# Kernel optimization log

Hardware: AMD Instinct MI355X
Metric: run time of the kernel (lower is better)

## Reference

```python
import jax, jax.numpy as jnp
import numpy as np

B, E, S, D = 32, 64, 50, 300   # batch, sentences/essay, words/sentence, word dim
F = 100                        # conv filters (cnn_lstm_convunits_size)
H = 100                        # lstm units (cnn_lstm_att_pool_size)
W_WIN = 5                      # word window length


def setup_inputs() -> dict:
    key = jax.random.key(0)
    ks = jax.random.split(key, 12)
    n = lambda k, shape: (jax.random.normal(k, shape, jnp.float32) * 0.05)
    return {
        "essays": jax.random.normal(ks[0], (B, E, S, D), jnp.float32),
        "conv_k": n(ks[1], (1, W_WIN, D, F)),      # HWIO
        "conv_b": jnp.zeros((F,), jnp.float32),
        "att1_mat": n(ks[2], (F, F)),
        "att1_bias": n(ks[3], (F,)),
        "att1_vec": n(ks[4], (F, 1)),
        "lstm_W": n(ks[5], (F + H, 4 * H)),        # TF BasicLSTMCell kernel, gate order i,j,f,o
        "lstm_b": jnp.zeros((4 * H,), jnp.float32),
        "att2_mat": n(ks[6], (H, H)),
        "att2_bias": n(ks[7], (H,)),
        "att2_vec": n(ks[8], (H, 1)),
        "dense_w": n(ks[9], (H, 1)),
        "dense_b": jnp.zeros((1,), jnp.float32),
    }


def reference(essays, conv_k, conv_b, att1_mat, att1_bias, att1_vec,
              lstm_W, lstm_b, att2_mat, att2_bias, att2_vec,
              dense_w, dense_b):
    # conv2d, kernel [1, w_window_len], SAME padding, relu  -> [B,E,S,F]
    conv1 = jax.lax.conv_general_dilated(
        essays, conv_k, window_strides=(1, 1), padding="SAME",
        dimension_numbers=("NHWC", "HWIO", "NHWC"))
    conv1 = jax.nn.relu(conv1 + conv_b)

    # attention pooling over words (axis=2)
    a1 = jnp.tanh(jnp.einsum("besf,fg->besg", conv1, att1_mat) + att1_bias)
    a1 = jnp.einsum("besg,go->beso", a1, att1_vec)          # [B,E,S,1]
    a1 = jax.nn.softmax(a1, axis=2)
    sent = jnp.sum(a1 * conv1, axis=2)                       # [B,E,F]

    # BasicLSTMCell (forget_bias=1.0, gate order i,j,f,o) over sentence axis
    hdim = lstm_b.shape[0] // 4
    bsz = essays.shape[0]

    def step(carry, xt):
        c, h = carry
        z = jnp.concatenate([xt, h], axis=1) @ lstm_W + lstm_b
        i, j, f, o = jnp.split(z, 4, axis=1)
        c = c * jax.nn.sigmoid(f + 1.0) + jax.nn.sigmoid(i) * jnp.tanh(j)
        h = jax.nn.sigmoid(o) * jnp.tanh(c)
        return (c, h), h

    init = (jnp.zeros((bsz, hdim), sent.dtype), jnp.zeros((bsz, hdim), sent.dtype))
    xs = jnp.swapaxes(sent, 0, 1)                            # [E,B,F]
    _, hs = jax.lax.scan(step, init, xs)
    lstm = jnp.swapaxes(hs, 0, 1)                            # [B,E,H]

    # attention pooling over sentences (axis=1)
    a2 = jnp.tanh(jnp.einsum("beh,hg->beg", lstm, att2_mat) + att2_bias)
    a2 = jnp.einsum("beg,go->beo", a2, att2_vec)             # [B,E,1]
    a2 = jax.nn.softmax(a2, axis=1)
    essay_repr = jnp.sum(a2 * lstm, axis=1)                  # [B,H]

    preds = jax.nn.sigmoid(essay_repr @ dense_w + dense_b).reshape(-1)  # [B]
    return preds
```

## Files before the change

kernel.cpp:

```cpp
#include <hip/hip_runtime.h>
#include <hip/hip_bf16.h>
#include <stdint.h>

#define Bsz 32
#define Esz 64
#define Ssz 50
#define Dsz 300
#define Fsz 100
#define Hsz 100
#define WWIN 5

#define PX   328
#define PC   136
#define KT_CONV 50
#define NTILES  7
#define MTILES  4
#define NGRP 2214

typedef __attribute__((ext_vector_type(8))) short bf16x8;
typedef __attribute__((ext_vector_type(8))) unsigned short u16x8;
typedef __attribute__((ext_vector_type(4))) float f32x4;
typedef _Float16 half2_t __attribute__((ext_vector_type(2)));

union UH32 { unsigned int u; half2_t v; };
union UH16 { _Float16 h; unsigned short u; };

__device__ __forceinline__ float sigmoid_fast(float x) {
    return 1.0f / (1.0f + __expf(-x));
}
__device__ __forceinline__ float tanhf_fast(float x) {
    const float ax = fabsf(x);
    const float e = __expf(2.0f * ax);
    const float t = 1.0f - 2.0f / (e + 1.0f);
    return copysignf(t, x);
}

__device__ __forceinline__ unsigned short f2bf(float x) {
    union { __hip_bfloat16 h; unsigned short u; } cv;
    cv.h = __float2bfloat16(x);
    return cv.u;
}
__device__ __forceinline__ unsigned int f2bf2(float lo, float hi) {
    union { __hip_bfloat162 h2; unsigned int u; } cv;
    cv.h2 = __float22bfloat162_rn(make_float2(lo, hi));
    return cv.u;
}
__device__ __forceinline__ float bf2f(unsigned short b) {
    union { uint32_t u; float f; } v; v.u = ((uint32_t)b) << 16;
    return v.f;
}
__device__ __forceinline__ float dpp_bcast(float z, const int sel) {
    int r;
    switch (sel) {
        case 0: r = __builtin_amdgcn_mov_dpp(__builtin_bit_cast(int, z), 0x00, 0xf, 0xf, false); break;
        case 1: r = __builtin_amdgcn_mov_dpp(__builtin_bit_cast(int, z), 0x55, 0xf, 0xf, false); break;
        case 2: r = __builtin_amdgcn_mov_dpp(__builtin_bit_cast(int, z), 0xaa, 0xf, 0xf, false); break;
        default: r = __builtin_amdgcn_mov_dpp(__builtin_bit_cast(int, z), 0xff, 0xf, 0xf, false); break;
    }
    return __builtin_bit_cast(float, r);
}

#define N_BTGC (KT_CONV * 112 * 32)
#define N_BTGA (4 * 112 * 32)
#define N_BTGW (4 * 400 * 32)
#define N_BTGP (52 * 400)

__global__ __launch_bounds__(256) void prep_kernel(
    const float* __restrict__ conv_k, const float* __restrict__ att1_mat,
    const float* __restrict__ lstm_W,
    unsigned short* __restrict__ BtgC, unsigned short* __restrict__ BtgA,
    unsigned short* __restrict__ BtgW, unsigned int* __restrict__ BtgP)
{
    const int total = N_BTGC + N_BTGA + N_BTGW + N_BTGP;
    for (int i = blockIdx.x * 256 + threadIdx.x; i < total; i += gridDim.x * 256) {
        if (i < N_BTGC) {
            const int kt = i / (112 * 32);
            const int r  = i % (112 * 32);
            const int n  = r / 32;
            const int kk = r % 32;
            const int w  = kt / 10;
            const int d  = (kt % 10) * 32 + kk;
            float val = (d < Dsz && n < Fsz) ? conv_k[((size_t)w * Dsz + d) * Fsz + n] : 0.f;
            BtgC[i] = f2bf(val);
        } else if (i < N_BTGC + N_BTGA) {
            const int j  = i - N_BTGC;
            const int kt = j / (112 * 32);
            const int r  = j % (112 * 32);
            const int n  = r / 32;
            const int kk = r % 32;
            const int k  = kt * 32 + kk;
            float val = (k < Fsz && n < Fsz) ? att1_mat[(size_t)k * Fsz + n] : 0.f;
            BtgA[j] = f2bf(val);
        } else if (i < N_BTGC + N_BTGA + N_BTGW) {
            const int j  = i - N_BTGC - N_BTGA;
            const int kt = j / (400 * 32);
            const int r  = j % (400 * 32);
            const int n  = r / 32;
            const int kk = r % 32;
            const int k  = kt * 32 + kk;
            float val = (k < Fsz) ? lstm_W[(size_t)k * 400 + n] : 0.f;
            BtgW[j] = f2bf(val);
        } else {
            const int j   = i - N_BTGC - N_BTGA - N_BTGW;
            const int k2  = j / 400;
            const int col = j - k2 * 400;
            const int gate = col & 3;
            const int cell = col >> 2;
            const int src  = gate * 100 + cell;
            const int k0 = 2 * k2, k1 = 2 * k2 + 1;
            const float v0 = (k0 < Hsz) ? lstm_W[(size_t)(Fsz + k0) * 400 + src] : 0.f;
            const float v1 = (k1 < Hsz) ? lstm_W[(size_t)(Fsz + k1) * 400 + src] : 0.f;
            union { _Float16 h[2]; unsigned int u; } cv;
            cv.h[0] = (_Float16)v0;
            cv.h[1] = (_Float16)v1;
            BtgP[j] = cv.u;
        }
    }
}

template<int G>
__device__ __forceinline__ void conv_loadB(
    const unsigned short* __restrict__ BtgC, int boff0, int boff1, bool has1,
    bf16x8 (&bR)[5][2])
{
#pragma unroll
    for (int i = 0; i < 5; ++i) {
        const int kt = G * 5 + i;
        bR[i][0] = *reinterpret_cast<const bf16x8*>(BtgC + kt * 3584 + boff0);
        bR[i][1] = has1 ? *reinterpret_cast<const bf16x8*>(BtgC + kt * 3584 + boff1)
                        : (bf16x8)0;
    }
}

template<int KT>
__device__ __forceinline__ void conv_loadA(
    const unsigned short* b0p, const unsigned short* b1p,
    const int (&abase)[MTILES], bf16x8 (&a)[2][MTILES])
{
    constexpr int w   = KT / 10;
    constexpr int t   = KT % 10;
    constexpr int off = w * PX + t * 32;
#pragma unroll
    for (int mt = 0; mt < MTILES; ++mt) {
        a[0][mt] = *reinterpret_cast<const bf16x8*>(&b0p[abase[mt] + off]);
        a[1][mt] = *reinterpret_cast<const bf16x8*>(&b1p[abase[mt] + off]);
    }
}

__device__ __forceinline__ void mfma16(
    const bf16x8 (&a)[2][MTILES], const bf16x8 (&b)[2], bool has1,
    f32x4 (&acc)[2][MTILES][2])
{
    __builtin_amdgcn_s_setprio(1);
#pragma unroll
    for (int es = 0; es < 2; ++es) {
#pragma unroll
        for (int mt = 0; mt < MTILES; ++mt) {
            acc[es][mt][0] = __builtin_amdgcn_mfma_f32_16x16x32_bf16(a[es][mt], b[0], acc[es][mt][0], 0, 0, 0);
            if (has1)
                acc[es][mt][1] = __builtin_amdgcn_mfma_f32_16x16x32_bf16(a[es][mt], b[1], acc[es][mt][1], 0, 0, 0);
        }
    }
    __builtin_amdgcn_s_setprio(0);
}

template<int KT>
__device__ __forceinline__ void conv_kt(
    const unsigned short* b0p, const unsigned short* b1p,
    const int (&abase)[MTILES], bool has1, const bf16x8 (&b)[2],
    bf16x8 (&aX)[2][MTILES], bf16x8 (&aY)[2][MTILES],
    f32x4 (&acc)[2][MTILES][2])
{
    constexpr bool even = (KT % 2) == 0;
    if constexpr (KT + 1 < KT_CONV) {
        if constexpr (even) conv_loadA<KT + 1>(b0p, b1p, abase, aY);
        else                conv_loadA<KT + 1>(b0p, b1p, abase, aX);
    }
    if constexpr (even) mfma16(aX, b, has1, acc);
    else                mfma16(aY, b, has1, acc);
}

template<int G>
__device__ __forceinline__ void conv_group(
    const unsigned short* b0p, const unsigned short* b1p,
    const int (&abase)[MTILES], bool has1, const bf16x8 (&bR)[5][2],
    bf16x8 (&aX)[2][MTILES], bf16x8 (&aY)[2][MTILES],
    f32x4 (&acc)[2][MTILES][2])
{
    conv_kt<G * 5 + 0>(b0p, b1p, abase, has1, bR[0], aX, aY, acc);
    conv_kt<G * 5 + 1>(b0p, b1p, abase, has1, bR[1], aX, aY, acc);
    conv_kt<G * 5 + 2>(b0p, b1p, abase, has1, bR[2], aX, aY, acc);
    conv_kt<G * 5 + 3>(b0p, b1p, abase, has1, bR[3], aX, aY, acc);
    conv_kt<G * 5 + 4>(b0p, b1p, abase, has1, bR[4], aX, aY, acc);
}

template<int KT>
__device__ __forceinline__ void att_loadA(
    const unsigned short* b0p, const unsigned short* b1p,
    const int (&abase2)[MTILES], bf16x8 (&a)[2][MTILES])
{
    constexpr int off = KT * 32;
#pragma unroll
    for (int mt = 0; mt < MTILES; ++mt) {
        a[0][mt] = *reinterpret_cast<const bf16x8*>(&b0p[abase2[mt] + off]);
        a[1][mt] = *reinterpret_cast<const bf16x8*>(&b1p[abase2[mt] + off]);
    }
}

__global__ __launch_bounds__(256, 2) void conv_att1_kernel(
    const float* __restrict__ essays,
    const unsigned short* __restrict__ BtgC,
    const unsigned short* __restrict__ BtgA,
    const float* __restrict__ conv_b,
    const float* __restrict__ att1_bias,
    const float* __restrict__ att1_vec,
    unsigned short* __restrict__ sent_bf)
{
    __shared__ __align__(16) unsigned short buf[2][54 * PX];
    __shared__ float u_s[2][64];
    __shared__ float alpha_s[2][64];

    const int be0 = blockIdx.x * 2;
    const int tid = threadIdx.x;
    const int lane = tid & 63;
    const int wid  = tid >> 6;
    const int ln   = lane & 15;
    const int qd   = lane >> 4;

    if (tid < 128) u_s[tid >> 6][tid & 63] = 0.f;

    const int nt0 = wid;
    const int nt1 = wid + 4;
    const bool has1 = (nt1 < NTILES);
    const int boff0 = (nt0 * 16 + ln) * 32 + 8 * qd;
    const int boff1 = (nt1 * 16 + ln) * 32 + 8 * qd;

    int abase[MTILES];
#pragma unroll
    for (int mt = 0; mt < MTILES; ++mt) {
        const int m = mt * 16 + ln;
        abase[mt] = (m < Ssz ? m : Ssz - 1) * PX + 8 * qd;
    }

    bf16x8 bX[5][2], bY[5][2];
    conv_loadB<0>(BtgC, boff0, boff1, has1, bX);
    conv_loadB<1>(BtgC, boff0, boff1, has1, bY);

#pragma unroll
    for (int es = 0; es < 2; ++es) {
        const float* in_g = essays + (size_t)(be0 + es) * (Ssz * Dsz);
        float4 va[9], vb[9];
        int rr[9], cc[9];
        bool hv[9], fv[9], gv[9];
#pragma unroll
        for (int it = 0; it < 9; ++it) {
            const int g  = tid + it * 256;
            const int r  = g / 41;
            const int c8 = (g - r * 41) * 8;
            const int s  = r - 2;
            gv[it] = (g < NGRP);
            hv[it] = gv[it] && (s >= 0) && (s < Ssz) && (c8 < Dsz);
            fv[it] = hv[it] && (c8 + 8 <= Dsz);
            const float* base = in_g + (hv[it] ? (s * Dsz + c8) : 0);
            va[it] = *reinterpret_cast<const float4*>(base);
            vb[it] = *reinterpret_cast<const float4*>(fv[it] ? base + 4 : base);
            rr[it] = r; cc[it] = c8;
        }
#pragma unroll
        for (int it = 0; it < 9; ++it) {
            if (!gv[it]) continue;
            const float e0 = hv[it] ? va[it].x : 0.f;
            const float e1 = hv[it] ? va[it].y : 0.f;
            const float e2 = hv[it] ? va[it].z : 0.f;
            const float e3 = hv[it] ? va[it].w : 0.f;
            const float e4 = fv[it] ? vb[it].x : 0.f;
            const float e5 = fv[it] ? vb[it].y : 0.f;
            const float e6 = fv[it] ? vb[it].z : 0.f;
            const float e7 = fv[it] ? vb[it].w : 0.f;
            uint4 o;
            o.x = f2bf2(e0, e1);
            o.y = f2bf2(e2, e3);
            o.z = f2bf2(e4, e5);
            o.w = f2bf2(e6, e7);
            *reinterpret_cast<uint4*>(&buf[es][rr[it] * PX + cc[it]]) = o;
        }
    }
    __syncthreads();

    const unsigned short* b0p = buf[0];
    const unsigned short* b1p = buf[1];

    f32x4 acc[2][MTILES][2];
#pragma unroll
    for (int es = 0; es < 2; ++es)
#pragma unroll
        for (int mt = 0; mt < MTILES; ++mt) { acc[es][mt][0] = (f32x4)0.f; acc[es][mt][1] = (f32x4)0.f; }

    {
        bf16x8 aX[2][MTILES], aY[2][MTILES];
        conv_loadA<0>(b0p, b1p, abase, aX);
        conv_group<0>(b0p, b1p, abase, has1, bX, aX, aY, acc);
        conv_loadB<2>(BtgC, boff0, boff1, has1, bX);
        conv_group<1>(b0p, b1p, abase, has1, bY, aX, aY, acc);
        conv_loadB<3>(BtgC, boff0, boff1, has1, bY);
        conv_group<2>(b0p, b1p, abase, has1, bX, aX, aY, acc);
        conv_loadB<4>(BtgC, boff0, boff1, has1, bX);
        conv_group<3>(b0p, b1p, abase, has1, bY, aX, aY, acc);
        conv_loadB<5>(BtgC, boff0, boff1, has1, bY);
        conv_group<4>(b0p, b1p, abase, has1, bX, aX, aY, acc);
        conv_loadB<6>(BtgC, boff0, boff1, has1, bX);
        conv_group<5>(b0p, b1p, abase, has1, bY, aX, aY, acc);
        conv_loadB<7>(BtgC, boff0, boff1, has1, bY);
        conv_group<6>(b0p, b1p, abase, has1, bX, aX, aY, acc);
        conv_loadB<8>(BtgC, boff0, boff1, has1, bX);
        conv_group<7>(b0p, b1p, abase, has1, bY, aX, aY, acc);
        conv_loadB<9>(BtgC, boff0, boff1, has1, bY);
        conv_group<8>(b0p, b1p, abase, has1, bX, aX, aY, acc);
        conv_group<9>(b0p, b1p, abase, has1, bY, aX, aY, acc);
    }

    bf16x8 a1b[4][2];
#pragma unroll
    for (int kt = 0; kt < 4; ++kt) {
        a1b[kt][0] = *reinterpret_cast<const bf16x8*>(BtgA + kt * 3584 + boff0);
        a1b[kt][1] = has1 ? *reinterpret_cast<const bf16x8*>(BtgA + kt * 3584 + boff1)
                          : (bf16x8)0;
    }
    __syncthreads();

    {
        const float bias0 = conv_b[nt0 * 16 + ln];
        const int n_g1 = nt1 * 16 + ln;
        const bool g1ok = has1 && (n_g1 < Fsz);
        const float bias1 = g1ok ? conv_b[n_g1] : 0.f;
#pragma unroll
        for (int es = 0; es < 2; ++es) {
#pragma unroll
            for (int mt = 0; mt < MTILES; ++mt) {
#pragma unroll
                for (int j = 0; j < 4; ++j) {
                    const int m_row = mt * 16 + qd * 4 + j;
                    buf[es][m_row * PC + nt0 * 16 + ln] = f2bf(fmaxf(acc[es][mt][0][j] + bias0, 0.f));
                    if (g1ok)
                        buf[es][m_row * PC + n_g1] = f2bf(fmaxf(acc[es][mt][1][j] + bias1, 0.f));
                }
            }
        }
    }
    for (int idx = tid; idx < 2 * 64 * 2; idx += 256) {
        const int es = idx >> 7;
        const int r2 = idx & 127;
        const int row = r2 >> 1;
        const int c = 112 + (r2 & 1) * 8;
        *reinterpret_cast<u16x8*>(&buf[es][row * PC + c]) = (u16x8)0;
    }
    __syncthreads();

    f32x4 acc2[2][MTILES][2];
#pragma unroll
    for (int es = 0; es < 2; ++es)
#pragma unroll
        for (int mt = 0; mt < MTILES; ++mt) { acc2[es][mt][0] = (f32x4)0.f; acc2[es][mt][1] = (f32x4)0.f; }

    {
        int abase2[MTILES];
#pragma unroll
        for (int mt = 0; mt < MTILES; ++mt) abase2[mt] = (mt * 16 + ln) * PC + 8 * qd;

        bf16x8 aX[2][MTILES], aY[2][MTILES];
        att_loadA<0>(b0p, b1p, abase2, aX);
        att_loadA<1>(b0p, b1p, abase2, aY);
        mfma16(aX, a1b[0], has1, acc2);
        att_loadA<2>(b0p, b1p, abase2, aX);
        mfma16(aY, a1b[1], has1, acc2);
        att_loadA<3>(b0p, b1p, abase2, aY);
        mfma16(aX, a1b[2], has1, acc2);
        mfma16(aY, a1b[3], has1, acc2);
    }

    {
        const int g0 = nt0 * 16 + ln;
        const float b1v0 = att1_bias[g0];
        const float vv0  = att1_vec[g0];
        const int g1 = nt1 * 16 + ln;
        const bool g1v = has1 && (g1 < Fsz);
        const float b1v1 = g1v ? att1_bias[g1] : 0.f;
        const float vv1  = g1v ? att1_vec[g1]  : 0.f;
#pragma unroll
        for (int es = 0; es < 2; ++es) {
#pragma unroll
            for (int mt = 0; mt < MTILES; ++mt) {
#pragma unroll
                for (int j = 0; j < 4; ++j) {
                    const int m_row = mt * 16 + qd * 4 + j;
                    float val = 0.f;
                    if (m_row < Ssz) {
                        val = tanhf_fast(acc2[es][mt][0][j] + b1v0) * vv0;
                        if (g1v) val += tanhf_fast(acc2[es][mt][1][j] + b1v1) * vv1;
                    }
                    val += __shfl_xor(val, 1);
                    val += __shfl_xor(val, 2);
                    val += __shfl_xor(val, 4);
                    val += __shfl_xor(val, 8);
                    if (ln == 0 && m_row < Ssz) atomicAdd(&u_s[es][m_row], val);
                }
            }
        }
    }
    __syncthreads();

    if (wid < 2) {
        const float uv = (lane < Ssz) ? u_s[wid][lane] : -1e30f;
        float m = uv;
#pragma unroll
        for (int off = 32; off > 0; off >>= 1) m = fmaxf(m, __shfl_xor(m, off));
        float e = (lane < Ssz) ? __expf(uv - m) : 0.f;
        float sum = e;
#pragma unroll
        for (int off = 32; off > 0; off >>= 1) sum += __shfl_xor(sum, off);
        alpha_s[wid][lane] = e / sum;
    }
    __syncthreads();

    {
        const int es = tid >> 7;
        const int f  = tid & 127;
        unsigned short v = 0;
        if (f < Fsz) {
            float a = 0.f;
            for (int s = 0; s < Ssz; ++s) a += alpha_s[es][s] * bf2f(buf[es][s * PC + f]);
            v = f2bf(a);
        }
        sent_bf[(size_t)(be0 + es) * 128 + f] = v;
    }
}

__global__ __launch_bounds__(256) void xpart_kernel(
    const unsigned short* __restrict__ sent_bf,
    const unsigned short* __restrict__ BtgW,
    const float* __restrict__ lstm_b,
    float* __restrict__ xpartB)
{
    const int wid  = threadIdx.x >> 6;
    const int mt   = blockIdx.x * 4 + wid;
    const int lane = threadIdx.x & 63;
    const int ln   = lane & 15;
    const int qd   = lane >> 4;
    const int m0   = mt * 16;

    f32x4 acc[25];
#pragma unroll
    for (int nt = 0; nt < 25; ++nt) acc[nt] = (f32x4)0.f;

#pragma unroll
    for (int kt = 0; kt < 4; ++kt) {
        const bf16x8 a = *reinterpret_cast<const bf16x8*>(
            sent_bf + (size_t)(m0 + ln) * 128 + kt * 32 + 8 * qd);
#pragma unroll
        for (int nt = 0; nt < 25; ++nt) {
            const bf16x8 b = *reinterpret_cast<const bf16x8*>(
                BtgW + ((size_t)kt * 400 + nt * 16 + ln) * 32 + 8 * qd);
            acc[nt] = __builtin_amdgcn_mfma_f32_16x16x32_bf16(a, b, acc[nt], 0, 0, 0);
        }
    }

#pragma unroll
    for (int nt = 0; nt < 25; ++nt) {
        const int col = nt * 16 + ln;
        const int gate = col / 100;
        const int cell = col - gate * 100;
        const float bias = lstm_b[col];
        const int gi = cell * 4 + gate;
#pragma unroll
        for (int j = 0; j < 4; ++j) {
            const int row = m0 + qd * 4 + j;
            xpartB[(size_t)row * 400 + gi] = acc[nt][j] + bias;
        }
    }
}

__global__ __launch_bounds__(448) void lstm_att2_kernel(
    const float* __restrict__ xpartB,
    const unsigned int* __restrict__ BtgP,
    const float* __restrict__ att2_mat,
    const float* __restrict__ att2_bias,
    const float* __restrict__ att2_vec,
    const float* __restrict__ dense_w,
    const float* __restrict__ dense_b,
    float* __restrict__ out)
{
    __shared__ __align__(16) float xp_lds[Esz * 400];
    __shared__ __align__(16) float hist[Esz * Hsz];
    __shared__ __align__(16) unsigned short h16[2][104];
    __shared__ float u2_s[Esz];
    __shared__ float alpha2_s[Esz];
    __shared__ float repr_s[Hsz];

    const int b   = blockIdx.x;
    const int tid = threadIdx.x;
    const bool actv = tid < 400;
    const int cell = tid >> 2;
    const int g    = tid & 3;

    {
        const float4* src = reinterpret_cast<const float4*>(xpartB + (size_t)b * Esz * 400);
        float4* dst = reinterpret_cast<float4*>(xp_lds);
        for (int i = tid; i < Esz * 100; i += 448) dst[i] = src[i];
    }

    unsigned int wp[52];
    if (actv) {
#pragma unroll
        for (int q = 0; q < 52; ++q) wp[q] = BtgP[q * 400 + tid];
    }
    if (tid < 104) { h16[0][tid] = 0; h16[1][tid] = 0; }
    float c = 0.f;
    __syncthreads();

    for (int t = 0; t < Esz; ++t) {
        float z = 0.f;
        if (actv) {
            const uint4* hq = reinterpret_cast<const uint4*>(h16[t & 1]);
            float za = xp_lds[t * 400 + tid], zb = 0.f, zc = 0.f, zd = 0.f;
#pragma unroll
            for (int q = 0; q < 13; ++q) {
                const uint4 hv = hq[q];
                UH32 h0, h1, h2, h3, w0, w1, w2, w3;
                h0.u = hv.x; h1.u = hv.y; h2.u = hv.z; h3.u = hv.w;
                w0.u = wp[4 * q + 0]; w1.u = wp[4 * q + 1];
                w2.u = wp[4 * q + 2]; w3.u = wp[4 * q + 3];
                za = __builtin_amdgcn_fdot2(w0.v, h0.v, za, false);
                zb = __builtin_amdgcn_fdot2(w1.v, h1.v, zb, false);
                zc = __builtin_amdgcn_fdot2(w2.v, h2.v, zc, false);
                zd = __builtin_amdgcn_fdot2(w3.v, h3.v, zd, false);
            }
            z = (za + zb) + (zc + zd);

            const float zi = dpp_bcast(z, 0);
            const float zj = dpp_bcast(z, 1);
            const float zf = dpp_bcast(z, 2);
            const float zo = dpp_bcast(z, 3);

            c = c * sigmoid_fast(zf + 1.0f) + sigmoid_fast(zi) * tanhf_fast(zj);
            const float h = sigmoid_fast(zo) * tanhf_fast(c);
            if (g == 0) {
                UH16 cv; cv.h = (_Float16)h;
                h16[(t + 1) & 1][cell] = cv.u;
                hist[t * Hsz + cell] = h;
            }
        }
        __syncthreads();
    }

    float* w2_s = xp_lds;
    for (int idx = tid; idx < Esz * Hsz; idx += 448) {
        const int e = idx / Hsz;
        const int gg = idx - e * Hsz;
        const float* lp = hist + e * Hsz;
        float a0 = 0.f, a1 = 0.f, a2 = 0.f, a3 = 0.f;
        for (int k = 0; k < Hsz; k += 4) {
            a0 += lp[k + 0] * att2_mat[(k + 0) * Hsz + gg];
            a1 += lp[k + 1] * att2_mat[(k + 1) * Hsz + gg];
            a2 += lp[k + 2] * att2_mat[(k + 2) * Hsz + gg];
            a3 += lp[k + 3] * att2_mat[(k + 3) * Hsz + gg];
        }
        w2_s[idx] = tanhf_fast(att2_bias[gg] + ((a0 + a1) + (a2 + a3))) * att2_vec[gg];
    }
    __syncthreads();

    if (tid < Esz) {
        float acc = 0.f;
        const float* wpp = w2_s + tid * Hsz;
        for (int gg = 0; gg < Hsz; ++gg) acc += wpp[gg];
        u2_s[tid] = acc;
    }
    __syncthreads();

    if (tid < 64) {
        const float uv = u2_s[tid];
        float m = uv;
#pragma unroll
        for (int off = 32; off > 0; off >>= 1) m = fmaxf(m, __shfl_xor(m, off));
        float e = __expf(uv - m);
        float sum = e;
#pragma unroll
        for (int off = 32; off > 0; off >>= 1) sum += __shfl_xor(sum, off);
        alpha2_s[tid] = e / sum;
    }
    __syncthreads();

    if (tid < Hsz) {
        float acc = 0.f;
        for (int e = 0; e < Esz; ++e) acc += alpha2_s[e] * hist[e * Hsz + tid];
        repr_s[tid] = acc;
    }
    __syncthreads();

    if (tid == 0) {
        float acc = dense_b[0];
        for (int hh = 0; hh < Hsz; ++hh) acc += repr_s[hh] * dense_w[hh];
        out[b] = sigmoid_fast(acc);
    }
}

extern "C" void kernel_launch(void* const* d_in, const int* in_sizes, int n_in,
                              void* d_out, int out_size, void* d_ws, size_t ws_size,
                              hipStream_t stream) {
    const float* essays    = (const float*)d_in[0];
    const float* conv_k    = (const float*)d_in[1];
    const float* conv_b    = (const float*)d_in[2];
    const float* att1_mat  = (const float*)d_in[3];
    const float* att1_bias = (const float*)d_in[4];
    const float* att1_vec  = (const float*)d_in[5];
    const float* lstm_W    = (const float*)d_in[6];
    const float* lstm_b    = (const float*)d_in[7];
    const float* att2_mat  = (const float*)d_in[8];
    const float* att2_bias = (const float*)d_in[9];
    const float* att2_vec  = (const float*)d_in[10];
    const float* dense_w   = (const float*)d_in[11];
    const float* dense_b   = (const float*)d_in[12];

    float* out = (float*)d_out;

    char* ws = (char*)d_ws;
    unsigned short* sent_bf = (unsigned short*)ws;
    float* xpartB = (float*)(ws + 524288);
    unsigned short* BtgC = (unsigned short*)(ws + 3801088);
    unsigned short* BtgA = (unsigned short*)(ws + 4159488);
    unsigned short* BtgW = (unsigned short*)(ws + 4188160);
    unsigned int*   BtgP = (unsigned int*)(ws + 4290560);

    prep_kernel<<<512, 256, 0, stream>>>(conv_k, att1_mat, lstm_W, BtgC, BtgA, BtgW, BtgP);
    conv_att1_kernel<<<Bsz * Esz / 2, 256, 0, stream>>>(
        essays, BtgC, BtgA, conv_b, att1_bias, att1_vec, sent_bf);
    xpart_kernel<<<32, 256, 0, stream>>>(sent_bf, BtgW, lstm_b, xpartB);
    lstm_att2_kernel<<<Bsz, 448, 0, stream>>>(
        xpartB, BtgP, att2_mat, att2_bias, att2_vec, dense_w, dense_b, out);
}
```

Before: 185.9 us.

## Repartition conv/att1 MFMA work so each wave owns one M-tile across all N-tiles

Each wave now computes one 16-row M-tile against all 7 N-tiles, instead of all 4 M-tiles against one or two N-tiles. This evens out work, since wave 3 previously had only one N-tile. It also cuts per-wave LDS A-fragment reads from eight to two per k-step. In exchange each wave must fetch all 7 B fragments per k-step from global memory. The B fetches go into a triple-buffered register ring prefetched two k-steps ahead through a recursive template unroll, which raises VGPR pressure.

```diff
diff --git a/kernel.cpp b/kernel.cpp
--- a/kernel.cpp
+++ b/kernel.cpp
@@ -14,7 +14,6 @@
 #define PC   136
 #define KT_CONV 50
 #define NTILES  7
-#define MTILES  4
 #define NGRP 2214
 
 typedef __attribute__((ext_vector_type(8))) short bf16x8;
@@ -118,94 +117,73 @@
     }
 }
 
-template<int G>
-__device__ __forceinline__ void conv_loadB(
-    const unsigned short* __restrict__ BtgC, int boff0, int boff1, bool has1,
-    bf16x8 (&bR)[5][2])
-{
-#pragma unroll
-    for (int i = 0; i < 5; ++i) {
-        const int kt = G * 5 + i;
-        bR[i][0] = *reinterpret_cast<const bf16x8*>(BtgC + kt * 3584 + boff0);
-        bR[i][1] = has1 ? *reinterpret_cast<const bf16x8*>(BtgC + kt * 3584 + boff1)
-                        : (bf16x8)0;
-    }
-}
-
 template<int KT>
-__device__ __forceinline__ void conv_loadA(
-    const unsigned short* b0p, const unsigned short* b1p,
-    const int (&abase)[MTILES], bf16x8 (&a)[2][MTILES])
-{
-    constexpr int w   = KT / 10;
-    constexpr int t   = KT % 10;
-    constexpr int off = w * PX + t * 32;
-#pragma unroll
-    for (int mt = 0; mt < MTILES; ++mt) {
-        a[0][mt] = *reinterpret_cast<const bf16x8*>(&b0p[abase[mt] + off]);
-        a[1][mt] = *reinterpret_cast<const bf16x8*>(&b1p[abase[mt] + off]);
-    }
-}
-
-__device__ __forceinline__ void mfma16(
-    const bf16x8 (&a)[2][MTILES], const bf16x8 (&b)[2], bool has1,
-    f32x4 (&acc)[2][MTILES][2])
+__device__ __forceinline__ void cv_loadB(
+    const unsigned short* __restrict__ BtgC, const int (&boffs)[7], bf16x8 (&b)[7])
+{
+#pragma unroll
+    for (int nt = 0; nt < 7; ++nt)
+        b[nt] = *reinterpret_cast<const bf16x8*>(BtgC + KT * 3584 + boffs[nt]);
+}
+
+template<int KT>
+__device__ __forceinline__ void cv_loadA(
+    const unsigned short* b0p, const unsigned short* b1p, int abase, bf16x8 (&a)[2])
+{
+    constexpr int off = (KT / 10) * PX + (KT % 10) * 32;
+    a[0] = *reinterpret_cast<const bf16x8*>(&b0p[abase + off]);
+    a[1] = *reinterpret_cast<const bf16x8*>(&b1p[abase + off]);
+}
+
+__device__ __forceinline__ void cv_mfma(
+    const bf16x8 (&a)[2], const bf16x8 (&b)[7], f32x4 (&acc)[2][7])
 {
     __builtin_amdgcn_s_setprio(1);
 #pragma unroll
-    for (int es = 0; es < 2; ++es) {
-#pragma unroll
-        for (int mt = 0; mt < MTILES; ++mt) {
-            acc[es][mt][0] = __builtin_amdgcn_mfma_f32_16x16x32_bf16(a[es][mt], b[0], acc[es][mt][0], 0, 0, 0);
-            if (has1)
-                acc[es][mt][1] = __builtin_amdgcn_mfma_f32_16x16x32_bf16(a[es][mt], b[1], acc[es][mt][1], 0, 0, 0);
-        }
+    for (int nt = 0; nt < 7; ++nt) {
+        acc[0][nt] = __builtin_amdgcn_mfma_f32_16x16x32_bf16(a[0], b[nt], acc[0][nt], 0, 0, 0);
+        acc[1][nt] = __builtin_amdgcn_mfma_f32_16x16x32_bf16(a[1], b[nt], acc[1][nt], 0, 0, 0);
     }
     __builtin_amdgcn_s_setprio(0);
 }
 
 template<int KT>
-__device__ __forceinline__ void conv_kt(
-    const unsigned short* b0p, const unsigned short* b1p,
-    const int (&abase)[MTILES], bool has1, const bf16x8 (&b)[2],
-    bf16x8 (&aX)[2][MTILES], bf16x8 (&aY)[2][MTILES],
-    f32x4 (&acc)[2][MTILES][2])
-{
-    constexpr bool even = (KT % 2) == 0;
-    if constexpr (KT + 1 < KT_CONV) {
-        if constexpr (even) conv_loadA<KT + 1>(b0p, b1p, abase, aY);
-        else                conv_loadA<KT + 1>(b0p, b1p, abase, aX);
-    }
-    if constexpr (even) mfma16(aX, b, has1, acc);
-    else                mfma16(aY, b, has1, acc);
-}
-
-template<int G>
-__device__ __forceinline__ void conv_group(
-    const unsigned short* b0p, const unsigned short* b1p,
-    const int (&abase)[MTILES], bool has1, const bf16x8 (&bR)[5][2],
-    bf16x8 (&aX)[2][MTILES], bf16x8 (&aY)[2][MTILES],
-    f32x4 (&acc)[2][MTILES][2])
-{
-    conv_kt<G * 5 + 0>(b0p, b1p, abase, has1, bR[0], aX, aY, acc);
-    conv_kt<G * 5 + 1>(b0p, b1p, abase, has1, bR[1], aX, aY, acc);
-    conv_kt<G * 5 + 2>(b0p, b1p, abase, has1, bR[2], aX, aY, acc);
-    conv_kt<G * 5 + 3>(b0p, b1p, abase, has1, bR[3], aX, aY, acc);
-    conv_kt<G * 5 + 4>(b0p, b1p, abase, has1, bR[4], aX, aY, acc);
-}
-
-template<int KT>
-__device__ __forceinline__ void att_loadA(
-    const unsigned short* b0p, const unsigned short* b1p,
-    const int (&abase2)[MTILES], bf16x8 (&a)[2][MTILES])
-{
-    constexpr int off = KT * 32;
-#pragma unroll
-    for (int mt = 0; mt < MTILES; ++mt) {
-        a[0][mt] = *reinterpret_cast<const bf16x8*>(&b0p[abase2[mt] + off]);
-        a[1][mt] = *reinterpret_cast<const bf16x8*>(&b1p[abase2[mt] + off]);
-    }
-}
+struct CvLoop {
+    static __device__ __forceinline__ void run(
+        const unsigned short* __restrict__ BtgC, const int (&boffs)[7],
+        const unsigned short* b0p, const unsigned short* b1p, int abase,
+        bf16x8 (&B0)[7], bf16x8 (&B1)[7], bf16x8 (&B2)[7],
+        bf16x8 (&aX)[2], bf16x8 (&aY)[2], f32x4 (&acc)[2][7])
+    {
+        if constexpr (KT + 1 < KT_CONV) {
+            if constexpr ((KT & 1) == 0) cv_loadA<KT + 1>(b0p, b1p, abase, aY);
+            else                         cv_loadA<KT + 1>(b0p, b1p, abase, aX);
+        }
+        if constexpr (KT + 2 < KT_CONV) {
+            if constexpr ((KT + 2) % 3 == 0)      cv_loadB<KT + 2>(BtgC, boffs, B0);
+            else if constexpr ((KT + 2) % 3 == 1) cv_loadB<KT + 2>(BtgC, boffs, B1);
+            else                                  cv_loadB<KT + 2>(BtgC, boffs, B2);
+        }
+        if constexpr ((KT & 1) == 0) {
+            if constexpr (KT % 3 == 0)      cv_mfma(aX, B0, acc);
+            else if constexpr (KT % 3 == 1) cv_mfma(aX, B1, acc);
+            else                            cv_mfma(aX, B2, acc);
+        } else {
+            if constexpr (KT % 3 == 0)      cv_mfma(aY, B0, acc);
+            else if constexpr (KT % 3 == 1) cv_mfma(aY, B1, acc);
+            else                            cv_mfma(aY, B2, acc);
+        }
+        CvLoop<KT + 1>::run(BtgC, boffs, b0p, b1p, abase, B0, B1, B2, aX, aY, acc);
+    }
+};
+template<>
+struct CvLoop<KT_CONV> {
+    static __device__ __forceinline__ void run(
+        const unsigned short* __restrict__, const int (&)[7],
+        const unsigned short*, const unsigned short*, int,
+        bf16x8 (&)[7], bf16x8 (&)[7], bf16x8 (&)[7],
+        bf16x8 (&)[2], bf16x8 (&)[2], f32x4 (&)[2][7]) {}
+};
 
 __global__ __launch_bounds__(256, 2) void conv_att1_kernel(
     const float* __restrict__ essays,
@@ -229,22 +207,16 @@
 
     if (tid < 128) u_s[tid >> 6][tid & 63] = 0.f;
 
-    const int nt0 = wid;
-    const int nt1 = wid + 4;
-    const bool has1 = (nt1 < NTILES);
-    const int boff0 = (nt0 * 16 + ln) * 32 + 8 * qd;
-    const int boff1 = (nt1 * 16 + ln) * 32 + 8 * qd;
-
-    int abase[MTILES];
-#pragma unroll
-    for (int mt = 0; mt < MTILES; ++mt) {
-        const int m = mt * 16 + ln;
-        abase[mt] = (m < Ssz ? m : Ssz - 1) * PX + 8 * qd;
-    }
-
-    bf16x8 bX[5][2], bY[5][2];
-    conv_loadB<0>(BtgC, boff0, boff1, has1, bX);
-    conv_loadB<1>(BtgC, boff0, boff1, has1, bY);
+    const int m = wid * 16 + ln;
+    const int abase = (m < Ssz ? m : Ssz - 1) * PX + 8 * qd;
+
+    int boffs[7];
+#pragma unroll
+    for (int nt = 0; nt < 7; ++nt) boffs[nt] = (nt * 16 + ln) * 32 + 8 * qd;
+
+    bf16x8 B0[7], B1[7], B2[7];
+    cv_loadB<0>(BtgC, boffs, B0);
+    cv_loadB<1>(BtgC, boffs, B1);
 
 #pragma unroll
     for (int es = 0; es < 2; ++es) {
@@ -290,60 +262,29 @@
     const unsigned short* b0p = buf[0];
     const unsigned short* b1p = buf[1];
 
-    f32x4 acc[2][MTILES][2];
+    f32x4 acc[2][7];
 #pragma unroll
     for (int es = 0; es < 2; ++es)
 #pragma unroll
-        for (int mt = 0; mt < MTILES; ++mt) { acc[es][mt][0] = (f32x4)0.f; acc[es][mt][1] = (f32x4)0.f; }
+        for (int nt = 0; nt < 7; ++nt) acc[es][nt] = (f32x4)0.f;
 
     {
-        bf16x8 aX[2][MTILES], aY[2][MTILES];
-        conv_loadA<0>(b0p, b1p, abase, aX);
-        conv_group<0>(b0p, b1p, abase, has1, bX, aX, aY, acc);
-        conv_loadB<2>(BtgC, boff0, boff1, has1, bX);
-        conv_group<1>(b0p, b1p, abase, has1, bY, aX, aY, acc);
-        conv_loadB<3>(BtgC, boff0, boff1, has1, bY);
-        conv_group<2>(b0p, b1p, abase, has1, bX, aX, aY, acc);
-        conv_loadB<4>(BtgC, boff0, boff1, has1, bX);
-        conv_group<3>(b0p, b1p, abase, has1, bY, aX, aY, acc);
-        conv_loadB<5>(BtgC, boff0, boff1, has1, bY);
-        conv_group<4>(b0p, b1p, abase, has1, bX, aX, aY, acc);
-        conv_loadB<6>(BtgC, boff0, boff1, has1, bX);
-        conv_group<5>(b0p, b1p, abase, has1, bY, aX, aY, acc);
-        conv_loadB<7>(BtgC, boff0, boff1, has1, bY);
-        conv_group<6>(b0p, b1p, abase, has1, bX, aX, aY, acc);
-        conv_loadB<8>(BtgC, boff0, boff1, has1, bX);
-        conv_group<7>(b0p, b1p, abase, has1, bY, aX, aY, acc);
-        conv_loadB<9>(BtgC, boff0, boff1, has1, bY);
-        conv_group<8>(b0p, b1p, abase, has1, bX, aX, aY, acc);
-        conv_group<9>(b0p, b1p, abase, has1, bY, aX, aY, acc);
-    }
-
-    bf16x8 a1b[4][2];
-#pragma unroll
-    for (int kt = 0; kt < 4; ++kt) {
-        a1b[kt][0] = *reinterpret_cast<const bf16x8*>(BtgA + kt * 3584 + boff0);
-        a1b[kt][1] = has1 ? *reinterpret_cast<const bf16x8*>(BtgA + kt * 3584 + boff1)
-                          : (bf16x8)0;
-    }
-    __syncthreads();
-
-    {
-        const float bias0 = conv_b[nt0 * 16 + ln];
-        const int n_g1 = nt1 * 16 + ln;
-        const bool g1ok = has1 && (n_g1 < Fsz);
-        const float bias1 = g1ok ? conv_b[n_g1] : 0.f;
+        bf16x8 aX[2], aY[2];
+        cv_loadA<0>(b0p, b1p, abase, aX);
+        CvLoop<0>::run(BtgC, boffs, b0p, b1p, abase, B0, B1, B2, aX, aY, acc);
+    }
+    __syncthreads();
+
+#pragma unroll
+    for (int nt = 0; nt < 7; ++nt) {
+        const int n_g = nt * 16 + ln;
+        const float bias = (n_g < Fsz) ? conv_b[n_g] : 0.f;
 #pragma unroll
         for (int es = 0; es < 2; ++es) {
 #pragma unroll
-            for (int mt = 0; mt < MTILES; ++mt) {
-#pragma unroll
-                for (int j = 0; j < 4; ++j) {
-                    const int m_row = mt * 16 + qd * 4 + j;
-                    buf[es][m_row * PC + nt0 * 16 + ln] = f2bf(fmaxf(acc[es][mt][0][j] + bias0, 0.f));
-                    if (g1ok)
-                        buf[es][m_row * PC + n_g1] = f2bf(fmaxf(acc[es][mt][1][j] + bias1, 0.f));
-                }
+            for (int j = 0; j < 4; ++j) {
+                const int m_row = wid * 16 + qd * 4 + j;
+                buf[es][m_row * PC + n_g] = f2bf(fmaxf(acc[es][nt][j] + bias, 0.f));
             }
         }
     }
@@ -356,54 +297,59 @@
     }
     __syncthreads();
 
-    f32x4 acc2[2][MTILES][2];
+    f32x4 acc2[2][7];
 #pragma unroll
     for (int es = 0; es < 2; ++es)
 #pragma unroll
-        for (int mt = 0; mt < MTILES; ++mt) { acc2[es][mt][0] = (f32x4)0.f; acc2[es][mt][1] = (f32x4)0.f; }
+        for (int nt = 0; nt < 7; ++nt) acc2[es][nt] = (f32x4)0.f;
+
+    const int abase2 = (wid * 16 + ln) * PC + 8 * qd;
+#pragma unroll
+    for (int kt = 0; kt < 4; ++kt) {
+        bf16x8 a[2];
+        a[0] = *reinterpret_cast<const bf16x8*>(&b0p[abase2 + kt * 32]);
+        a[1] = *reinterpret_cast<const bf16x8*>(&b1p[abase2 + kt * 32]);
+        bf16x8 bb[7];
+#pragma unroll
+        for (int nt = 0; nt < 7; ++nt)
+            bb[nt] = *reinterpret_cast<const bf16x8*>(BtgA + kt * 3584 + boffs[nt]);
+        __builtin_amdgcn_s_setprio(1);
+#pragma unroll
+        for (int nt = 0; nt < 7; ++nt) {
+            acc2[0][nt] = __builtin_amdgcn_mfma_f32_16x16x32_bf16(a[0], bb[nt], acc2[0][nt], 0, 0, 0);
+            acc2[1][nt] = __builtin_amdgcn_mfma_f32_16x16x32_bf16(a[1], bb[nt], acc2[1][nt], 0, 0, 0);
+        }
+        __builtin_amdgcn_s_setprio(0);
+    }
 
     {
-        int abase2[MTILES];
-#pragma unroll
-        for (int mt = 0; mt < MTILES; ++mt) abase2[mt] = (mt * 16 + ln) * PC + 8 * qd;
-
-        bf16x8 aX[2][MTILES], aY[2][MTILES];
-        att_loadA<0>(b0p, b1p, abase2, aX);
-        att_loadA<1>(b0p, b1p, abase2, aY);
-        mfma16(aX, a1b[0], has1, acc2);
-        att_loadA<2>(b0p, b1p, abase2, aX);
-        mfma16(aY, a1b[1], has1, acc2);
-        att_loadA<3>(b0p, b1p, abase2, aY);
-        mfma16(aX, a1b[2], has1, acc2);
-        mfma16(aY, a1b[3], has1, acc2);
-    }
-
-    {
-        const int g0 = nt0 * 16 + ln;
-        const float b1v0 = att1_bias[g0];
-        const float vv0  = att1_vec[g0];
-        const int g1 = nt1 * 16 + ln;
-        const bool g1v = has1 && (g1 < Fsz);
-        const float b1v1 = g1v ? att1_bias[g1] : 0.f;
-        const float vv1  = g1v ? att1_vec[g1]  : 0.f;
+        float bias_v[7], vec_v[7];
+#pragma unroll
+        for (int nt = 0; nt < 7; ++nt) {
+            const int g = nt * 16 + ln;
+            const bool ok = (g < Fsz);
+            bias_v[nt] = ok ? att1_bias[g] : 0.f;
+            vec_v[nt]  = ok ? att1_vec[g]  : 0.f;
+        }
 #pragma unroll
         for (int es = 0; es < 2; ++es) {
 #pragma unroll
-            for (int mt = 0; mt < MTILES; ++mt) {
-#pragma unroll
-                for (int j = 0; j < 4; ++j) {
-                    const int m_row = mt * 16 + qd * 4 + j;
-                    float val = 0.f;
-                    if (m_row < Ssz) {
-                        val = tanhf_fast(acc2[es][mt][0][j] + b1v0) * vv0;
-                        if (g1v) val += tanhf_fast(acc2[es][mt][1][j] + b1v1) * vv1;
+            for (int j = 0; j < 4; ++j) {
+                const int m_row = wid * 16 + qd * 4 + j;
+                float val = 0.f;
+                if (m_row < Ssz) {
+#pragma unroll
+                    for (int nt = 0; nt < 7; ++nt) {
+                        const int g = nt * 16 + ln;
+                        if (g < Fsz)
+                            val += tanhf_fast(acc2[es][nt][j] + bias_v[nt]) * vec_v[nt];
                     }
-                    val += __shfl_xor(val, 1);
-                    val += __shfl_xor(val, 2);
-                    val += __shfl_xor(val, 4);
-                    val += __shfl_xor(val, 8);
-                    if (ln == 0 && m_row < Ssz) atomicAdd(&u_s[es][m_row], val);
                 }
+                val += __shfl_xor(val, 1);
+                val += __shfl_xor(val, 2);
+                val += __shfl_xor(val, 4);
+                val += __shfl_xor(val, 8);
+                if (ln == 0 && m_row < Ssz) atomicAdd(&u_s[es][m_row], val);
             }
         }
     }
@@ -411,10 +357,10 @@
 
     if (wid < 2) {
         const float uv = (lane < Ssz) ? u_s[wid][lane] : -1e30f;
-        float m = uv;
-#pragma unroll
-        for (int off = 32; off > 0; off >>= 1) m = fmaxf(m, __shfl_xor(m, off));
-        float e = (lane < Ssz) ? __expf(uv - m) : 0.f;
+        float m2 = uv;
+#pragma unroll
+        for (int off = 32; off > 0; off >>= 1) m2 = fmaxf(m2, __shfl_xor(m2, off));
+        float e = (lane < Ssz) ? __expf(uv - m2) : 0.f;
         float sum = e;
 #pragma unroll
         for (int off = 32; off > 0; off >>= 1) sum += __shfl_xor(sum, off);
```

New measurement: 223.9 us. 1.2x slower.

## Compute two LSTM gates per thread to halve recurrent block size

Applied to the files above, without the earlier changes.

The LSTM recurrence kernel now has each thread compute two gate pre-activations instead of one. Blocks shrink from 448 to 256 threads (200 active), and weights are loaded as uint2 pairs. Gate exchange uses a single DPP pair swap rather than four quad broadcasts. The aim is a cheaper per-step __syncthreads across fewer wavefronts and shorter cross-lane traffic on the serial 64-step path. In exchange each thread does twice the dot-product work per step and holds twice the weight registers.

```diff
diff --git a/kernel.cpp b/kernel.cpp
--- a/kernel.cpp
+++ b/kernel.cpp
@@ -49,14 +49,8 @@
     union { uint32_t u; float f; } v; v.u = ((uint32_t)b) << 16;
     return v.f;
 }
-__device__ __forceinline__ float dpp_bcast(float z, const int sel) {
-    int r;
-    switch (sel) {
-        case 0: r = __builtin_amdgcn_mov_dpp(__builtin_bit_cast(int, z), 0x00, 0xf, 0xf, false); break;
-        case 1: r = __builtin_amdgcn_mov_dpp(__builtin_bit_cast(int, z), 0x55, 0xf, 0xf, false); break;
-        case 2: r = __builtin_amdgcn_mov_dpp(__builtin_bit_cast(int, z), 0xaa, 0xf, 0xf, false); break;
-        default: r = __builtin_amdgcn_mov_dpp(__builtin_bit_cast(int, z), 0xff, 0xf, 0xf, false); break;
-    }
+__device__ __forceinline__ float dpp_swap_pair(float z) {
+    int r = __builtin_amdgcn_mov_dpp(__builtin_bit_cast(int, z), 0xB1, 0xf, 0xf, false);
     return __builtin_bit_cast(float, r);
 }
 
@@ -479,7 +473,7 @@
     }
 }
 
-__global__ __launch_bounds__(448) void lstm_att2_kernel(
+__global__ __launch_bounds__(256, 1) void lstm_att2_kernel(
     const float* __restrict__ xpartB,
     const unsigned int* __restrict__ BtgP,
     const float* __restrict__ att2_mat,
@@ -498,52 +492,64 @@
 
     const int b   = blockIdx.x;
     const int tid = threadIdx.x;
-    const bool actv = tid < 400;
-    const int cell = tid >> 2;
-    const int g    = tid & 3;
+    const bool actv = tid < 200;
+    const bool odd = tid & 1;
+    const int cell = tid >> 1;
 
     {
         const float4* src = reinterpret_cast<const float4*>(xpartB + (size_t)b * Esz * 400);
         float4* dst = reinterpret_cast<float4*>(xp_lds);
-        for (int i = tid; i < Esz * 100; i += 448) dst[i] = src[i];
-    }
-
-    unsigned int wp[52];
+        for (int i = tid; i < Esz * 100; i += 256) dst[i] = src[i];
+    }
+
+    uint2 wq[52];
     if (actv) {
 #pragma unroll
-        for (int q = 0; q < 52; ++q) wp[q] = BtgP[q * 400 + tid];
+        for (int q = 0; q < 52; ++q)
+            wq[q] = *reinterpret_cast<const uint2*>(BtgP + q * 400 + 2 * tid);
     }
     if (tid < 104) { h16[0][tid] = 0; h16[1][tid] = 0; }
     float c = 0.f;
     __syncthreads();
 
     for (int t = 0; t < Esz; ++t) {
-        float z = 0.f;
         if (actv) {
+            const float2 xp2 = *reinterpret_cast<const float2*>(&xp_lds[t * 400 + 2 * tid]);
             const uint4* hq = reinterpret_cast<const uint4*>(h16[t & 1]);
-            float za = xp_lds[t * 400 + tid], zb = 0.f, zc = 0.f, zd = 0.f;
+            float za0 = xp2.x, za1 = 0.f;
+            float zb0 = xp2.y, zb1 = 0.f;
 #pragma unroll
             for (int q = 0; q < 13; ++q) {
                 const uint4 hv = hq[q];
-                UH32 h0, h1, h2, h3, w0, w1, w2, w3;
+                UH32 h0, h1, h2, h3;
                 h0.u = hv.x; h1.u = hv.y; h2.u = hv.z; h3.u = hv.w;
-                w0.u = wp[4 * q + 0]; w1.u = wp[4 * q + 1];
-                w2.u = wp[4 * q + 2]; w3.u = wp[4 * q + 3];
-                za = __builtin_amdgcn_fdot2(w0.v, h0.v, za, false);
-                zb = __builtin_amdgcn_fdot2(w1.v, h1.v, zb, false);
-                zc = __builtin_amdgcn_fdot2(w2.v, h2.v, zc, false);
-                zd = __builtin_amdgcn_fdot2(w3.v, h3.v, zd, false);
+                UH32 wa0, wa1, wa2, wa3, wb0, wb1, wb2, wb3;
+                wa0.u = wq[4 * q + 0].x; wb0.u = wq[4 * q + 0].y;
+                wa1.u = wq[4 * q + 1].x; wb1.u = wq[4 * q + 1].y;
+                wa2.u = wq[4 * q + 2].x; wb2.u = wq[4 * q + 2].y;
+                wa3.u = wq[4 * q + 3].x; wb3.u = wq[4 * q + 3].y;
+                za0 = __builtin_amdgcn_fdot2(wa0.v, h0.v, za0, false);
+                za1 = __builtin_amdgcn_fdot2(wa1.v, h1.v, za1, false);
+                za0 = __builtin_amdgcn_fdot2(wa2.v, h2.v, za0, false);
+                za1 = __builtin_amdgcn_fdot2(wa3.v, h3.v, za1, false);
+                zb0 = __builtin_amdgcn_fdot2(wb0.v, h0.v, zb0, false);
+                zb1 = __builtin_amdgcn_fdot2(wb1.v, h1.v, zb1, false);
+                zb0 = __builtin_amdgcn_fdot2(wb2.v, h2.v, zb0, false);
+                zb1 = __builtin_amdgcn_fdot2(wb3.v, h3.v, zb1, false);
             }
-            z = (za + zb) + (zc + zd);
-
-            const float zi = dpp_bcast(z, 0);
-            const float zj = dpp_bcast(z, 1);
-            const float zf = dpp_bcast(z, 2);
-            const float zo = dpp_bcast(z, 3);
+            const float z0 = za0 + za1;
+            const float z1 = zb0 + zb1;
+
+            const float o0 = dpp_swap_pair(z0);
+            const float o1 = dpp_swap_pair(z1);
+            const float zi = odd ? o0 : z0;
+            const float zj = odd ? o1 : z1;
+            const float zf = odd ? z0 : o0;
+            const float zo = odd ? z1 : o1;
 
             c = c * sigmoid_fast(zf + 1.0f) + sigmoid_fast(zi) * tanhf_fast(zj);
             const float h = sigmoid_fast(zo) * tanhf_fast(c);
-            if (g == 0) {
+            if (!odd) {
                 UH16 cv; cv.h = (_Float16)h;
                 h16[(t + 1) & 1][cell] = cv.u;
                 hist[t * Hsz + cell] = h;
@@ -553,7 +559,7 @@
     }
 
     float* w2_s = xp_lds;
-    for (int idx = tid; idx < Esz * Hsz; idx += 448) {
+    for (int idx = tid; idx < Esz * Hsz; idx += 256) {
         const int e = idx / Hsz;
         const int gg = idx - e * Hsz;
         const float* lp = hist + e * Hsz;
@@ -634,6 +640,6 @@
     conv_att1_kernel<<<Bsz * Esz / 2, 256, 0, stream>>>(
         essays, BtgC, BtgA, conv_b, att1_bias, att1_vec, sent_bf);
     xpart_kernel<<<32, 256, 0, stream>>>(sent_bf, BtgW, lstm_b, xpartB);
-    lstm_att2_kernel<<<Bsz, 448, 0, stream>>>(
+    lstm_att2_kernel<<<Bsz, 256, 0, stream>>>(
         xpartB, BtgP, att2_mat, att2_bias, att2_vec, dense_w, dense_b, out);
 }
```

Result: slower. 192.1 us (+3.3%).
